# Kernel optimization log

Hardware: AMD Instinct MI355X
Metric: run time of the kernel (lower is better)

Reference implementation:

```python
import jax, jax.numpy as jnp
import numpy as np

B, I, H, O = 4096, 1024, 2048, 512  # batch, input_size, experts_out(hidden), experts_hidden(output)
E_SPEC, E_SH = 4, 4


def _experts(x, W1, b1, W2, b2):
    # x:[B,I], W1:[E,I,H], b1:[E,H], W2:[E,H,O], b2:[E,O] -> [E,B,O]
    # Expert: fc2(dropout(relu(fc1(x)))); dropout is identity in eval mode.
    h = jax.nn.relu(jnp.einsum('bi,eih->ebh', x, W1) + b1[:, None, :])
    return jnp.einsum('ebh,eho->ebo', h, W2) + b2[:, None, :]


def setup_inputs() -> dict:
    key = jax.random.key(0)
    ks = jax.random.split(key, 32)
    s = 0.02
    d = {}
    d['x_shared'] = jax.random.normal(ks[0], (B, I), jnp.float32)
    d['x_task1'] = jax.random.normal(ks[1], (B, I), jnp.float32)
    d['x_task2'] = jax.random.normal(ks[2], (B, I), jnp.float32)
    # expert params for shared / task1 / task2 groups
    for n, (grp, kbase) in enumerate([('sh', 3), ('t1', 8), ('t2', 13)]):
        E = E_SH if grp == 'sh' else E_SPEC
        d[f'w1_{grp}'] = jax.random.normal(ks[kbase], (E, I, H), jnp.float32) * s
        d[f'b1_{grp}'] = jnp.zeros((E, H), jnp.float32)
        d[f'w2_{grp}'] = jax.random.normal(ks[kbase + 1], (E, H, O), jnp.float32) * s
        d[f'b2_{grp}'] = jnp.zeros((E, O), jnp.float32)
    # gate params
    d['wg_sh'] = jax.random.normal(ks[20], (I, 2 * E_SPEC + E_SH), jnp.float32) * s
    d['bg_sh'] = jnp.zeros((2 * E_SPEC + E_SH,), jnp.float32)
    d['wg_t1'] = jax.random.normal(ks[21], (I, E_SPEC + E_SH), jnp.float32) * s
    d['bg_t1'] = jnp.zeros((E_SPEC + E_SH,), jnp.float32)
    d['wg_t2'] = jax.random.normal(ks[22], (I, E_SPEC + E_SH), jnp.float32) * s
    d['bg_t2'] = jnp.zeros((E_SPEC + E_SH,), jnp.float32)
    return d


def reference(x_shared, x_task1, x_task2,
              w1_sh, b1_sh, w2_sh, b2_sh,
              w1_t1, b1_t1, w2_t1, b2_t1,
              w1_t2, b1_t2, w2_t2, b2_t2,
              wg_sh, bg_sh, wg_t1, bg_t1, wg_t2, bg_t2):
    sh_o = _experts(x_shared, w1_sh, b1_sh, w2_sh, b2_sh)  # [Esh,B,O]
    t1_o = _experts(x_task1, w1_t1, b1_t1, w2_t1, b2_t1)   # [Esp,B,O]
    t2_o = _experts(x_task2, w1_t2, b1_t2, w2_t2, b2_t2)   # [Esp,B,O]

    g1 = jax.nn.softmax(x_task1 @ wg_t1 + bg_t1, axis=1)    # [B,Esp+Esh]
    g2 = jax.nn.softmax(x_task2 @ wg_t2 + bg_t2, axis=1)
    gs = jax.nn.softmax(x_shared @ wg_sh + bg_sh, axis=1)   # [B,2Esp+Esh]

    out1 = jnp.einsum('ebc,be->bc', jnp.concatenate([t1_o, sh_o], 0), g1)
    out2 = jnp.einsum('ebc,be->bc', jnp.concatenate([t2_o, sh_o], 0), g2)
    out_sh = jnp.einsum('ebc,be->bc', jnp.concatenate([t1_o, t2_o, sh_o], 0), gs)
    # if_last=False -> return [shared, task1, task2]
    return (out_sh, out1, out2)
```

## Files before the change

### kernel.cpp

```cpp
#include <hip/hip_runtime.h>

#define B_DIM 4096
#define I_DIM 1024
#define H_DIM 2048
#define O_DIM 512

typedef unsigned short ushort_t;
typedef unsigned long long ull_t;
typedef __attribute__((ext_vector_type(4))) float f32x4;
typedef __attribute__((ext_vector_type(8))) short bf16x8;
typedef __attribute__((ext_vector_type(8))) unsigned short u16x8;
typedef __attribute__((ext_vector_type(4))) unsigned short u16x4;

__device__ __forceinline__ unsigned short f2bf(float f) {
  union { float f; unsigned int u; } v; v.f = f;
  unsigned int u = v.u;
  u += 0x7fffu + ((u >> 16) & 1u);
  return (unsigned short)(u >> 16);
}
__device__ __forceinline__ float bf2f(unsigned short h) {
  union { unsigned int u; float f; } v; v.u = ((unsigned int)h) << 16;
  return v.f;
}

__device__ __forceinline__ void gld16(const void* g, void* l) {
  __builtin_amdgcn_global_load_lds(
      (const __attribute__((address_space(1))) unsigned int*)((ull_t)g),
      (__attribute__((address_space(3))) unsigned int*)((unsigned int)(ull_t)l),
      16, 0, 0);
}

__device__ __forceinline__ int swz_off(int row, int col) {
  int off = ((((row >> 4) << 1) + (col >> 5)) << 10) + ((row & 15) << 6) + ((col & 31) << 1);
  off ^= ((row >> 3) & 1) << 5;
  return off;
}

template <bool RELU>
__device__ __forceinline__ void gemm_core_256(
    const ushort_t* __restrict__ A,
    const ushort_t* __restrict__ Bt,
    const float*    __restrict__ bias,
    ushort_t*       __restrict__ C,
    int N, int K, int bm0, int bn0)
{
  __shared__ __align__(16) ushort_t sh[2][2][16384];

  const int tid  = threadIdx.x;
  const int lane = tid & 63;
  const int wave = tid >> 6;
  const int wm = wave >> 2, wn = wave & 3;
  const int r16 = lane & 15, kq = lane >> 4;

  int   loff[4];
  ull_t goffA[4], goffB[4];
#pragma unroll
  for (int r = 0; r < 4; ++r) {
    const int L = (r * 512 + tid) * 16;
    const int P = L ^ (((L >> 9) & 1) << 5);
    const int s = P >> 10;
    const int row = ((s >> 1) << 4) | ((P >> 6) & 15);
    const int col = ((s & 1) << 5) | (((P >> 4) & 3) << 3);
    loff[r]  = L;
    goffA[r] = (ull_t)(bm0 + row) * K + col;
    goffB[r] = (ull_t)(bn0 + row) * K + col;
  }
  const int NT = K >> 6;

  int offA[8][2], offB[4][2];
#pragma unroll
  for (int m = 0; m < 8; ++m)
#pragma unroll
    for (int ks = 0; ks < 2; ++ks)
      offA[m][ks] = swz_off(wm * 128 + m * 16 + r16, ks * 32 + kq * 8);
#pragma unroll
  for (int n = 0; n < 4; ++n)
#pragma unroll
    for (int ks = 0; ks < 2; ++ks)
      offB[n][ks] = swz_off(wn * 64 + n * 16 + r16, ks * 32 + kq * 8);

  f32x4 acc[8][4] = {};

  auto stageA = [&](int b, int kt) {
    const int k0 = kt << 6;
    char* baseA = (char*)&sh[b][0][0];
#pragma unroll
    for (int r = 0; r < 4; ++r) gld16(A + goffA[r] + k0, baseA + loff[r]);
  };
  auto stageB = [&](int b, int kt) {
    const int k0 = kt << 6;
    char* baseB = (char*)&sh[b][1][0];
#pragma unroll
    for (int r = 0; r < 4; ++r) gld16(Bt + goffB[r] + k0, baseB + loff[r]);
  };

  stageA(0, 0); stageB(0, 0);
  stageA(1, 1); stageB(1, 1);

  for (int kt = 0; kt < NT; ++kt) {
    const int b = kt & 1;
    const bool pre = (kt + 2 < NT);
    if (kt < NT - 1) asm volatile("s_waitcnt vmcnt(8)" ::: "memory");
    else             asm volatile("s_waitcnt vmcnt(0)" ::: "memory");
    __builtin_amdgcn_s_barrier();

    const char* tA = (const char*)&sh[b][0][0];
    const char* tB = (const char*)&sh[b][1][0];

    bf16x8 a0[4][2], a1[4][2], bf0[2][2], bf1[2][2];

#pragma unroll
    for (int m = 0; m < 4; ++m) {
      a0[m][0] = *(const bf16x8*)(tA + offA[m][0]);
      a0[m][1] = *(const bf16x8*)(tA + offA[m][1]);
    }
#pragma unroll
    for (int n = 0; n < 2; ++n) {
      bf0[n][0] = *(const bf16x8*)(tB + offB[n][0]);
      bf0[n][1] = *(const bf16x8*)(tB + offB[n][1]);
    }
    asm volatile("" ::: "memory");
    __builtin_amdgcn_s_barrier();
    asm volatile("s_waitcnt lgkmcnt(0)" ::: "memory");
    __builtin_amdgcn_sched_barrier(0);
    __builtin_amdgcn_s_setprio(1);
#pragma unroll
    for (int m = 0; m < 4; ++m)
#pragma unroll
      for (int n = 0; n < 2; ++n)
#pragma unroll
        for (int ks = 0; ks < 2; ++ks)
          acc[m][n] = __builtin_amdgcn_mfma_f32_16x16x32_bf16(a0[m][ks], bf0[n][ks], acc[m][n], 0, 0, 0);
    __builtin_amdgcn_s_setprio(0);
    asm volatile("" ::: "memory");
    __builtin_amdgcn_s_barrier();

#pragma unroll
    for (int n = 0; n < 2; ++n) {
      bf1[n][0] = *(const bf16x8*)(tB + offB[n + 2][0]);
      bf1[n][1] = *(const bf16x8*)(tB + offB[n + 2][1]);
    }
    asm volatile("" ::: "memory");
    __builtin_amdgcn_s_barrier();
    asm volatile("s_waitcnt lgkmcnt(0)" ::: "memory");
    __builtin_amdgcn_sched_barrier(0);
    __builtin_amdgcn_s_setprio(1);
#pragma unroll
    for (int m = 0; m < 4; ++m)
#pragma unroll
      for (int n = 0; n < 2; ++n)
#pragma unroll
        for (int ks = 0; ks < 2; ++ks)
          acc[m][n + 2] = __builtin_amdgcn_mfma_f32_16x16x32_bf16(a0[m][ks], bf1[n][ks], acc[m][n + 2], 0, 0, 0);
    __builtin_amdgcn_s_setprio(0);
    asm volatile("" ::: "memory");
    __builtin_amdgcn_s_barrier();

#pragma unroll
    for (int m = 0; m < 4; ++m) {
      a1[m][0] = *(const bf16x8*)(tA + offA[m + 4][0]);
      a1[m][1] = *(const bf16x8*)(tA + offA[m + 4][1]);
    }
    if (pre) stageB(b, kt + 2);
    asm volatile("" ::: "memory");
    __builtin_amdgcn_s_barrier();
    asm volatile("s_waitcnt lgkmcnt(0)" ::: "memory");
    __builtin_amdgcn_sched_barrier(0);
    __builtin_amdgcn_s_setprio(1);
#pragma unroll
    for (int m = 0; m < 4; ++m)
#pragma unroll
      for (int n = 0; n < 2; ++n)
#pragma unroll
        for (int ks = 0; ks < 2; ++ks)
          acc[m + 4][n + 2] = __builtin_amdgcn_mfma_f32_16x16x32_bf16(a1[m][ks], bf1[n][ks], acc[m + 4][n + 2], 0, 0, 0);
    __builtin_amdgcn_s_setprio(0);
    asm volatile("" ::: "memory");
    __builtin_amdgcn_s_barrier();

    if (pre) stageA(b, kt + 2);
    asm volatile("" ::: "memory");
    __builtin_amdgcn_s_barrier();
    __builtin_amdgcn_sched_barrier(0);
    __builtin_amdgcn_s_setprio(1);
#pragma unroll
    for (int m = 0; m < 4; ++m)
#pragma unroll
      for (int n = 0; n < 2; ++n)
#pragma unroll
        for (int ks = 0; ks < 2; ++ks)
          acc[m + 4][n] = __builtin_amdgcn_mfma_f32_16x16x32_bf16(a1[m][ks], bf0[n][ks], acc[m + 4][n], 0, 0, 0);
    __builtin_amdgcn_s_setprio(0);
    asm volatile("" ::: "memory");
    __builtin_amdgcn_s_barrier();
  }

  float bv[4];
#pragma unroll
  for (int n = 0; n < 4; ++n) bv[n] = bias[bn0 + wn * 64 + n * 16 + r16];
#pragma unroll
  for (int m = 0; m < 8; ++m) {
    const int row = bm0 + wm * 128 + m * 16 + kq * 4;
#pragma unroll
    for (int n = 0; n < 4; ++n) {
      const int col = bn0 + wn * 64 + n * 16 + r16;
#pragma unroll
      for (int j = 0; j < 4; ++j) {
        float v = acc[m][n][j] + bv[n];
        if (RELU) v = fmaxf(v, 0.f);
        C[(ull_t)(row + j) * N + col] = f2bf(v);
      }
    }
  }
}

__device__ __forceinline__ void xcd_swz(int& bx, int& by, int& bz) {
  const int gx = gridDim.x, gy = gridDim.y;
  const int total = gx * gy * gridDim.z;
  const int flat = blockIdx.x + gx * (blockIdx.y + gy * blockIdx.z);
  const int q = total >> 3;
  const int s = (flat & 7) * q + (flat >> 3);
  bx = s % gx;
  const int rest = s / gx;
  by = rest % gy;
  bz = rest / gy;
}

__global__ __launch_bounds__(512, 2) void gemm1_256_kernel(
    const ushort_t* __restrict__ xb,
    const ushort_t* __restrict__ w1t,
    const float* __restrict__ b1_t1, const float* __restrict__ b1_t2, const float* __restrict__ b1_sh,
    ushort_t* __restrict__ hbuf,
    int ebase)
{
  int bx, by, bz; xcd_swz(bx, by, bz);
  const int eg = ebase + bz;
  const ushort_t* A  = xb + (ull_t)(eg >> 2) * B_DIM * I_DIM;
  const ushort_t* Bt = w1t + (ull_t)bz * H_DIM * I_DIM;
  const float* bias = (eg < 4 ? b1_t1 : eg < 8 ? b1_t2 : b1_sh) + (ull_t)(eg & 3) * H_DIM;
  ushort_t* C = hbuf + (ull_t)bz * B_DIM * H_DIM;
  gemm_core_256<true>(A, Bt, bias, C, H_DIM, I_DIM, by * 256, bx * 256);
}

__global__ __launch_bounds__(512, 2) void gemm2_256_kernel(
    const ushort_t* __restrict__ hbuf,
    const ushort_t* __restrict__ w2t,
    const float* __restrict__ b2_t1, const float* __restrict__ b2_t2, const float* __restrict__ b2_sh,
    ushort_t* __restrict__ eout,
    int ebase)
{
  int bx, by, bz; xcd_swz(bx, by, bz);
  const int eg = ebase + bz;
  const ushort_t* A  = hbuf + (ull_t)bz * B_DIM * H_DIM;
  const ushort_t* Bt = w2t + (ull_t)bz * O_DIM * H_DIM;
  const float* bias = (eg < 4 ? b2_t1 : eg < 8 ? b2_t2 : b2_sh) + (ull_t)(eg & 3) * O_DIM;
  ushort_t* C = eout + (ull_t)eg * B_DIM * O_DIM;
  gemm_core_256<false>(A, Bt, bias, C, O_DIM, H_DIM, by * 256, bx * 256);
}

__global__ void tcast_kernel(const float* __restrict__ s_t1, const float* __restrict__ s_t2,
                             const float* __restrict__ s_sh, ushort_t* __restrict__ dst,
                             int R, int C, int ebase)
{
  __shared__ float tile[32][33];
  const int eg = ebase + blockIdx.z;
  const float* src = (eg < 4 ? s_t1 : eg < 8 ? s_t2 : s_sh) + (ull_t)(eg & 3) * R * C;
  ushort_t* d = dst + (ull_t)blockIdx.z * R * C;
  const int tx = threadIdx.x, ty = threadIdx.y;
  const int r0 = blockIdx.y * 32, c0 = blockIdx.x * 32;
#pragma unroll
  for (int i = 0; i < 32; i += 8)
    tile[ty + i][tx] = src[(ull_t)(r0 + ty + i) * C + c0 + tx];
  __syncthreads();
#pragma unroll
  for (int i = 0; i < 32; i += 8)
    d[(ull_t)(c0 + ty + i) * R + r0 + tx] = f2bf(tile[tx][ty + i]);
}

__global__ void cast_x_kernel(const float* __restrict__ xt1, const float* __restrict__ xt2,
                              const float* __restrict__ xsh, ushort_t* __restrict__ dst)
{
  const int slot = blockIdx.y;
  const float* src = slot == 0 ? xt1 : slot == 1 ? xt2 : xsh;
  const ull_t base = ((ull_t)blockIdx.x * 256 + threadIdx.x) * 8;
  const f32x4* s4 = (const f32x4*)(src + base);
  f32x4 a = s4[0], b = s4[1];
  u16x8 r;
  r[0] = f2bf(a[0]); r[1] = f2bf(a[1]); r[2] = f2bf(a[2]); r[3] = f2bf(a[3]);
  r[4] = f2bf(b[0]); r[5] = f2bf(b[1]); r[6] = f2bf(b[2]); r[7] = f2bf(b[3]);
  *(u16x8*)(dst + (ull_t)slot * B_DIM * I_DIM + base) = r;
}

__global__ void prep_gates_w_kernel(const float* __restrict__ wg_sh, const float* __restrict__ wg_t1,
                                    const float* __restrict__ wg_t2, ushort_t* __restrict__ wgtb)
{
  const int t = blockIdx.x;
  const float* src = t == 0 ? wg_sh : t == 1 ? wg_t1 : wg_t2;
  const int n = t == 0 ? 12 : 8;
  ushort_t* dst = wgtb + (ull_t)t * 16 * I_DIM;
  for (int i = threadIdx.x; i < 16 * (I_DIM / 8); i += blockDim.x) {
    const int c = i >> 7, j0 = (i & 127) * 8;
    u16x8 r;
#pragma unroll
    for (int k = 0; k < 8; ++k)
      r[k] = (c < n) ? f2bf(src[(ull_t)(j0 + k) * n + c]) : (ushort_t)0;
    *(u16x8*)(dst + (ull_t)c * I_DIM + j0) = r;
  }
}

__global__ __launch_bounds__(256, 2) void gates_mfma_kernel(
    const ushort_t* __restrict__ xb, const ushort_t* __restrict__ wgtb,
    const float* __restrict__ bg_sh, const float* __restrict__ bg_t1, const float* __restrict__ bg_t2,
    float* __restrict__ gates)
{
  __shared__ __align__(16) ushort_t As[128 * 32];
  const int task = blockIdx.y;
  const int slot = task == 0 ? 2 : task - 1;
  const int n = task == 0 ? 12 : 8;
  const float* bg = task == 0 ? bg_sh : task == 1 ? bg_t1 : bg_t2;
  float* out = task == 0 ? gates
             : task == 1 ? gates + (ull_t)B_DIM * 12
                         : gates + (ull_t)B_DIM * 20;
  const ushort_t* A  = xb + (ull_t)slot * B_DIM * I_DIM;
  const ushort_t* Bt = wgtb + (ull_t)task * 16 * I_DIM;

  const int tid = threadIdx.x, lane = tid & 63, wave = tid >> 6;
  const int brow = blockIdx.x * 128;
  const int r16 = lane & 15, kq = lane >> 4;

  f32x4 acc[2] = {};
  const int c0 = tid, c1 = tid + 256;
  const ull_t a_off0 = (ull_t)(brow + (c0 >> 2)) * I_DIM + (c0 & 3) * 8;
  const ull_t a_off1 = (ull_t)(brow + (c1 >> 2)) * I_DIM + (c1 & 3) * 8;

  for (int k0 = 0; k0 < I_DIM; k0 += 32) {
    gld16(A + a_off0 + k0, As + c0 * 8);
    gld16(A + a_off1 + k0, As + c1 * 8);
    __syncthreads();
    const bf16x8 bfr = *(const bf16x8*)(Bt + (ull_t)r16 * I_DIM + k0 + kq * 8);
    const bf16x8 af0 = *(const bf16x8*)(As + (wave * 32 + r16) * 32 + kq * 8);
    const bf16x8 af1 = *(const bf16x8*)(As + (wave * 32 + 16 + r16) * 32 + kq * 8);
    acc[0] = __builtin_amdgcn_mfma_f32_16x16x32_bf16(af0, bfr, acc[0], 0, 0, 0);
    acc[1] = __builtin_amdgcn_mfma_f32_16x16x32_bf16(af1, bfr, acc[1], 0, 0, 0);
    __syncthreads();
  }

  const float bv = (r16 < n) ? bg[r16] : 0.f;
#pragma unroll
  for (int m = 0; m < 2; ++m) {
#pragma unroll
    for (int j = 0; j < 4; ++j) {
      float v = (r16 < n) ? (acc[m][j] + bv) : -1e30f;
      float mx = v;
#pragma unroll
      for (int d = 1; d < 16; d <<= 1) mx = fmaxf(mx, __shfl_xor(mx, d));
      const float e = __expf(v - mx);
      float s = e;
#pragma unroll
      for (int d = 1; d < 16; d <<= 1) s += __shfl_xor(s, d);
      const int row = brow + wave * 32 + m * 16 + kq * 4 + j;
      if (r16 < n) out[(ull_t)row * n + r16] = e / s;
    }
  }
}

__global__ __launch_bounds__(256) void combine_kernel(
    const ushort_t* __restrict__ eout, const float* __restrict__ gates, float* __restrict__ out)
{
  const ull_t idx4 = (ull_t)blockIdx.x * 256 + threadIdx.x;
  const int b  = (int)(idx4 >> 7);
  const int o4 = ((int)idx4 & 127) * 4;
  const float* gs = gates + (ull_t)b * 12;
  const float* g1 = gates + (ull_t)B_DIM * 12 + (ull_t)b * 8;
  const float* g2 = gates + (ull_t)B_DIM * 20 + (ull_t)b * 8;
  float osh[4] = {0, 0, 0, 0}, o1[4] = {0, 0, 0, 0}, o2[4] = {0, 0, 0, 0};
#pragma unroll
  for (int j = 0; j < 12; ++j) {
    const u16x4 ev = *(const u16x4*)(eout + ((ull_t)j * B_DIM + b) * O_DIM + o4);
    const float wsh = gs[j];
    const float w1 = (j < 4) ? g1[j] : (j >= 8 ? g1[j - 4] : 0.f);
    const float w2 = (j < 4) ? 0.f : g2[j - 4];
#pragma unroll
    for (int t = 0; t < 4; ++t) {
      const float e = bf2f(ev[t]);
      osh[t] += wsh * e; o1[t] += w1 * e; o2[t] += w2 * e;
    }
  }
  const ull_t nBO = (ull_t)B_DIM * O_DIM;
  const ull_t obase = (ull_t)b * O_DIM + o4;
  f32x4 v0 = {osh[0], osh[1], osh[2], osh[3]};
  f32x4 v1 = {o1[0], o1[1], o1[2], o1[3]};
  f32x4 v2 = {o2[0], o2[1], o2[2], o2[3]};
  *(f32x4*)(out + obase) = v0;
  *(f32x4*)(out + nBO + obase) = v1;
  *(f32x4*)(out + 2 * nBO + obase) = v2;
}

extern "C" void kernel_launch(void* const* d_in, const int* in_sizes, int n_in,
                              void* d_out, int out_size, void* d_ws, size_t ws_size,
                              hipStream_t stream)
{
  const float* x_sh  = (const float*)d_in[0];
  const float* x_t1  = (const float*)d_in[1];
  const float* x_t2  = (const float*)d_in[2];
  const float* w1_sh = (const float*)d_in[3];
  const float* b1_sh = (const float*)d_in[4];
  const float* w2_sh = (const float*)d_in[5];
  const float* b2_sh = (const float*)d_in[6];
  const float* w1_t1 = (const float*)d_in[7];
  const float* b1_t1 = (const float*)d_in[8];
  const float* w2_t1 = (const float*)d_in[9];
  const float* b2_t1 = (const float*)d_in[10];
  const float* w1_t2 = (const float*)d_in[11];
  const float* b1_t2 = (const float*)d_in[12];
  const float* w2_t2 = (const float*)d_in[13];
  const float* b2_t2 = (const float*)d_in[14];
  const float* wg_sh = (const float*)d_in[15];
  const float* bg_sh = (const float*)d_in[16];
  const float* wg_t1 = (const float*)d_in[17];
  const float* bg_t1 = (const float*)d_in[18];
  const float* wg_t2 = (const float*)d_in[19];
  const float* bg_t2 = (const float*)d_in[20];

  char* p = (char*)d_ws;
  auto alloc = [&](size_t bytes) { char* r = p; p += (bytes + 255) & ~(size_t)255; return r; };

  ushort_t* xb    = (ushort_t*)alloc(3ull * B_DIM * I_DIM * 2);
  ushort_t* eout  = (ushort_t*)alloc(12ull * B_DIM * O_DIM * 2);
  float*    gates = (float*)alloc(28ull * B_DIM * 4);
  ushort_t* wgtb  = (ushort_t*)alloc(3ull * 16 * I_DIM * 2);

  const size_t used_fixed = (size_t)(p - (char*)d_ws);
  const size_t per_e = ((size_t)H_DIM * I_DIM + (size_t)O_DIM * H_DIM + (size_t)B_DIM * H_DIM) * 2 + 3 * 256;
  int eb = 1;
  if (ws_size > used_fixed + per_e) eb = (int)((ws_size - used_fixed) / per_e);
  if (eb > 12) eb = 12;
  if (eb < 1)  eb = 1;

  ushort_t* w1t  = (ushort_t*)alloc((size_t)eb * H_DIM * I_DIM * 2);
  ushort_t* w2t  = (ushort_t*)alloc((size_t)eb * O_DIM * H_DIM * 2);
  ushort_t* hbuf = (ushort_t*)alloc((size_t)eb * B_DIM * H_DIM * 2);

  cast_x_kernel<<<dim3(2048, 3), 256, 0, stream>>>(x_t1, x_t2, x_sh, xb);
  prep_gates_w_kernel<<<3, 256, 0, stream>>>(wg_sh, wg_t1, wg_t2, wgtb);
  gates_mfma_kernel<<<dim3(B_DIM / 128, 3), 256, 0, stream>>>(xb, wgtb, bg_sh, bg_t1, bg_t2, gates);
  for (int ebase = 0; ebase < 12; ebase += eb) {
    const int cnt = (12 - ebase < eb) ? (12 - ebase) : eb;
    tcast_kernel<<<dim3(H_DIM / 32, I_DIM / 32, cnt), dim3(32, 8), 0, stream>>>(
        w1_t1, w1_t2, w1_sh, w1t, I_DIM, H_DIM, ebase);
    tcast_kernel<<<dim3(O_DIM / 32, H_DIM / 32, cnt), dim3(32, 8), 0, stream>>>(
        w2_t1, w2_t2, w2_sh, w2t, H_DIM, O_DIM, ebase);
    gemm1_256_kernel<<<dim3(H_DIM / 256, B_DIM / 256, cnt), 512, 0, stream>>>(
        xb, w1t, b1_t1, b1_t2, b1_sh, hbuf, ebase);
    gemm2_256_kernel<<<dim3(O_DIM / 256, B_DIM / 256, cnt), 512, 0, stream>>>(
        hbuf, w2t, b2_t1, b2_t2, b2_sh, eout, ebase);
  }
  combine_kernel<<<dim3((B_DIM * O_DIM / 4) / 256), 256, 0, stream>>>(eout, gates, (float*)d_out);
}
```

Measured before the change: 443.2 us.

## Templatize GEMM tiles, use 256x128 tiles for gemm2, vectorize transpose-cast stores

Turns the GEMM core into a template over the wave grid and per-wave MFMA repeats, so gemm2 can use 256x128 tiles (a 4x2 wave grid) and launch twice as many blocks. With only 512 output columns, the old 256x256 tiling gave gemm2 few blocks. The weight transpose-cast kernel now handles 64-row tiles and writes 16-byte vector stores instead of scalar 2-byte stores. In exchange, gemm2 re-reads each A tile more often and its LDS and register footprint changes.

```diff
diff --git a/kernel.cpp b/kernel.cpp
--- a/kernel.cpp
+++ b/kernel.cpp
@@ -36,62 +36,81 @@
   return off;
 }
 
-template <bool RELU>
-__device__ __forceinline__ void gemm_core_256(
+template <bool RELU, int WM, int WN, int MR, int NR>
+__device__ __forceinline__ void gemm_core(
     const ushort_t* __restrict__ A,
     const ushort_t* __restrict__ Bt,
     const float*    __restrict__ bias,
     ushort_t*       __restrict__ C,
     int N, int K, int bm0, int bn0)
 {
-  __shared__ __align__(16) ushort_t sh[2][2][16384];
+  constexpr int BM = WM * MR * 16;
+  constexpr int BN = WN * NR * 16;
+  constexpr int CA = BM / 64;
+  constexpr int CB = BN / 64;
+  constexpr int NTH = WM * WN * 64;
+  constexpr int MH = MR / 2, NH = NR / 2;
+  constexpr int ABYTES = BM * 128;
+  constexpr int BBYTES = BN * 128;
+  constexpr int VM = CA + CB;
+
+  __shared__ __align__(16) char lds[2 * (ABYTES + BBYTES)];
 
   const int tid  = threadIdx.x;
   const int lane = tid & 63;
   const int wave = tid >> 6;
-  const int wm = wave >> 2, wn = wave & 3;
+  const int wm = wave / WN, wn = wave % WN;
   const int r16 = lane & 15, kq = lane >> 4;
 
-  int   loff[4];
-  ull_t goffA[4], goffB[4];
-#pragma unroll
-  for (int r = 0; r < 4; ++r) {
-    const int L = (r * 512 + tid) * 16;
+  int loffA[CA]; ull_t goffA[CA];
+  int loffB[CB]; ull_t goffB[CB];
+#pragma unroll
+  for (int r = 0; r < CA; ++r) {
+    const int L = (r * NTH + tid) * 16;
     const int P = L ^ (((L >> 9) & 1) << 5);
     const int s = P >> 10;
     const int row = ((s >> 1) << 4) | ((P >> 6) & 15);
     const int col = ((s & 1) << 5) | (((P >> 4) & 3) << 3);
-    loff[r]  = L;
+    loffA[r] = L;
     goffA[r] = (ull_t)(bm0 + row) * K + col;
+  }
+#pragma unroll
+  for (int r = 0; r < CB; ++r) {
+    const int L = (r * NTH + tid) * 16;
+    const int P = L ^ (((L >> 9) & 1) << 5);
+    const int s = P >> 10;
+    const int row = ((s >> 1) << 4) | ((P >> 6) & 15);
+    const int col = ((s & 1) << 5) | (((P >> 4) & 3) << 3);
+    loffB[r] = L;
     goffB[r] = (ull_t)(bn0 + row) * K + col;
   }
   const int NT = K >> 6;
 
-  int offA[8][2], offB[4][2];
-#pragma unroll
-  for (int m = 0; m < 8; ++m)
+  int offA[MR][2], offB[NR][2];
+#pragma unroll
+  for (int m = 0; m < MR; ++m)
 #pragma unroll
     for (int ks = 0; ks < 2; ++ks)
-      offA[m][ks] = swz_off(wm * 128 + m * 16 + r16, ks * 32 + kq * 8);
-#pragma unroll
-  for (int n = 0; n < 4; ++n)
+      offA[m][ks] = swz_off(wm * MR * 16 + m * 16 + r16, ks * 32 + kq * 8);
+#pragma unroll
+  for (int n = 0; n < NR; ++n)
 #pragma unroll
     for (int ks = 0; ks < 2; ++ks)
-      offB[n][ks] = swz_off(wn * 64 + n * 16 + r16, ks * 32 + kq * 8);
-
-  f32x4 acc[8][4] = {};
+      offB[n][ks] = swz_off(wn * NR * 16 + n * 16 + r16, ks * 32 + kq * 8);
+
+  f32x4 acc[MR][NR] = {};
 
   auto stageA = [&](int b, int kt) {
+    char* base = lds + b * (ABYTES + BBYTES);
     const int k0 = kt << 6;
-    char* baseA = (char*)&sh[b][0][0];
-#pragma unroll
-    for (int r = 0; r < 4; ++r) gld16(A + goffA[r] + k0, baseA + loff[r]);
+#pragma unroll
+    for (int r = 0; r < CA; ++r) gld16(A + goffA[r] + k0, base + loffA[r]);
   };
   auto stageB = [&](int b, int kt) {
+    char* base = lds + b * (ABYTES + BBYTES) + ABYTES;
     const int k0 = kt << 6;
-    char* baseB = (char*)&sh[b][1][0];
-#pragma unroll
-    for (int r = 0; r < 4; ++r) gld16(Bt + goffB[r] + k0, baseB + loff[r]);
+#pragma unroll
+    for (int r = 0; r < CB; ++r) gld16(Bt + goffB[r] + k0, base + loffB[r]);
   };
 
   stageA(0, 0); stageB(0, 0);
@@ -100,24 +119,27 @@
   for (int kt = 0; kt < NT; ++kt) {
     const int b = kt & 1;
     const bool pre = (kt + 2 < NT);
-    if (kt < NT - 1) asm volatile("s_waitcnt vmcnt(8)" ::: "memory");
-    else             asm volatile("s_waitcnt vmcnt(0)" ::: "memory");
-    __builtin_amdgcn_s_barrier();
-
-    const char* tA = (const char*)&sh[b][0][0];
-    const char* tB = (const char*)&sh[b][1][0];
-
-    bf16x8 a0[4][2], a1[4][2], bf0[2][2], bf1[2][2];
-
-#pragma unroll
-    for (int m = 0; m < 4; ++m) {
-      a0[m][0] = *(const bf16x8*)(tA + offA[m][0]);
-      a0[m][1] = *(const bf16x8*)(tA + offA[m][1]);
-    }
-#pragma unroll
-    for (int n = 0; n < 2; ++n) {
-      bf0[n][0] = *(const bf16x8*)(tB + offB[n][0]);
-      bf0[n][1] = *(const bf16x8*)(tB + offB[n][1]);
+    if (kt < NT - 1) {
+      if constexpr (VM == 8)      asm volatile("s_waitcnt vmcnt(8)" ::: "memory");
+      else if constexpr (VM == 6) asm volatile("s_waitcnt vmcnt(6)" ::: "memory");
+      else                        asm volatile("s_waitcnt vmcnt(0)" ::: "memory");
+    } else                        asm volatile("s_waitcnt vmcnt(0)" ::: "memory");
+    __builtin_amdgcn_s_barrier();
+
+    const char* tA = lds + b * (ABYTES + BBYTES);
+    const char* tB = tA + ABYTES;
+
+    bf16x8 a_lo[MH][2], a_hi[MH][2], b_lo[NH][2], b_hi[NH][2];
+
+#pragma unroll
+    for (int m = 0; m < MH; ++m) {
+      a_lo[m][0] = *(const bf16x8*)(tA + offA[m][0]);
+      a_lo[m][1] = *(const bf16x8*)(tA + offA[m][1]);
+    }
+#pragma unroll
+    for (int n = 0; n < NH; ++n) {
+      b_lo[n][0] = *(const bf16x8*)(tB + offB[n][0]);
+      b_lo[n][1] = *(const bf16x8*)(tB + offB[n][1]);
     }
     asm volatile("" ::: "memory");
     __builtin_amdgcn_s_barrier();
@@ -125,20 +147,20 @@
     __builtin_amdgcn_sched_barrier(0);
     __builtin_amdgcn_s_setprio(1);
 #pragma unroll
-    for (int m = 0; m < 4; ++m)
-#pragma unroll
-      for (int n = 0; n < 2; ++n)
+    for (int m = 0; m < MH; ++m)
+#pragma unroll
+      for (int n = 0; n < NH; ++n)
 #pragma unroll
         for (int ks = 0; ks < 2; ++ks)
-          acc[m][n] = __builtin_amdgcn_mfma_f32_16x16x32_bf16(a0[m][ks], bf0[n][ks], acc[m][n], 0, 0, 0);
+          acc[m][n] = __builtin_amdgcn_mfma_f32_16x16x32_bf16(a_lo[m][ks], b_lo[n][ks], acc[m][n], 0, 0, 0);
     __builtin_amdgcn_s_setprio(0);
     asm volatile("" ::: "memory");
     __builtin_amdgcn_s_barrier();
 
 #pragma unroll
-    for (int n = 0; n < 2; ++n) {
-      bf1[n][0] = *(const bf16x8*)(tB + offB[n + 2][0]);
-      bf1[n][1] = *(const bf16x8*)(tB + offB[n + 2][1]);
+    for (int n = 0; n < NH; ++n) {
+      b_hi[n][0] = *(const bf16x8*)(tB + offB[n + NH][0]);
+      b_hi[n][1] = *(const bf16x8*)(tB + offB[n + NH][1]);
     }
     asm volatile("" ::: "memory");
     __builtin_amdgcn_s_barrier();
@@ -146,20 +168,20 @@
     __builtin_amdgcn_sched_barrier(0);
     __builtin_amdgcn_s_setprio(1);
 #pragma unroll
-    for (int m = 0; m < 4; ++m)
-#pragma unroll
-      for (int n = 0; n < 2; ++n)
+    for (int m = 0; m < MH; ++m)
+#pragma unroll
+      for (int n = 0; n < NH; ++n)
 #pragma unroll
         for (int ks = 0; ks < 2; ++ks)
-          acc[m][n + 2] = __builtin_amdgcn_mfma_f32_16x16x32_bf16(a0[m][ks], bf1[n][ks], acc[m][n + 2], 0, 0, 0);
+          acc[m][n + NH] = __builtin_amdgcn_mfma_f32_16x16x32_bf16(a_lo[m][ks], b_hi[n][ks], acc[m][n + NH], 0, 0, 0);
     __builtin_amdgcn_s_setprio(0);
     asm volatile("" ::: "memory");
     __builtin_amdgcn_s_barrier();
 
 #pragma unroll
-    for (int m = 0; m < 4; ++m) {
-      a1[m][0] = *(const bf16x8*)(tA + offA[m + 4][0]);
-      a1[m][1] = *(const bf16x8*)(tA + offA[m + 4][1]);
+    for (int m = 0; m < MH; ++m) {
+      a_hi[m][0] = *(const bf16x8*)(tA + offA[m + MH][0]);
+      a_hi[m][1] = *(const bf16x8*)(tA + offA[m + MH][1]);
     }
     if (pre) stageB(b, kt + 2);
     asm volatile("" ::: "memory");
@@ -168,12 +190,12 @@
     __builtin_amdgcn_sched_barrier(0);
     __builtin_amdgcn_s_setprio(1);
 #pragma unroll
-    for (int m = 0; m < 4; ++m)
-#pragma unroll
-      for (int n = 0; n < 2; ++n)
+    for (int m = 0; m < MH; ++m)
+#pragma unroll
+      for (int n = 0; n < NH; ++n)
 #pragma unroll
         for (int ks = 0; ks < 2; ++ks)
-          acc[m + 4][n + 2] = __builtin_amdgcn_mfma_f32_16x16x32_bf16(a1[m][ks], bf1[n][ks], acc[m + 4][n + 2], 0, 0, 0);
+          acc[m + MH][n + NH] = __builtin_amdgcn_mfma_f32_16x16x32_bf16(a_hi[m][ks], b_hi[n][ks], acc[m + MH][n + NH], 0, 0, 0);
     __builtin_amdgcn_s_setprio(0);
     asm volatile("" ::: "memory");
     __builtin_amdgcn_s_barrier();
@@ -184,26 +206,26 @@
     __builtin_amdgcn_sched_barrier(0);
     __builtin_amdgcn_s_setprio(1);
 #pragma unroll
-    for (int m = 0; m < 4; ++m)
-#pragma unroll
-      for (int n = 0; n < 2; ++n)
+    for (int m = 0; m < MH; ++m)
+#pragma unroll
+      for (int n = 0; n < NH; ++n)
 #pragma unroll
         for (int ks = 0; ks < 2; ++ks)
-          acc[m + 4][n] = __builtin_amdgcn_mfma_f32_16x16x32_bf16(a1[m][ks], bf0[n][ks], acc[m + 4][n], 0, 0, 0);
+          acc[m + MH][n] = __builtin_amdgcn_mfma_f32_16x16x32_bf16(a_hi[m][ks], b_lo[n][ks], acc[m + MH][n], 0, 0, 0);
     __builtin_amdgcn_s_setprio(0);
     asm volatile("" ::: "memory");
     __builtin_amdgcn_s_barrier();
   }
 
-  float bv[4];
-#pragma unroll
-  for (int n = 0; n < 4; ++n) bv[n] = bias[bn0 + wn * 64 + n * 16 + r16];
-#pragma unroll
-  for (int m = 0; m < 8; ++m) {
-    const int row = bm0 + wm * 128 + m * 16 + kq * 4;
-#pragma unroll
-    for (int n = 0; n < 4; ++n) {
-      const int col = bn0 + wn * 64 + n * 16 + r16;
+  float bv[NR];
+#pragma unroll
+  for (int n = 0; n < NR; ++n) bv[n] = bias[bn0 + wn * NR * 16 + n * 16 + r16];
+#pragma unroll
+  for (int m = 0; m < MR; ++m) {
+    const int row = bm0 + wm * MR * 16 + m * 16 + kq * 4;
+#pragma unroll
+    for (int n = 0; n < NR; ++n) {
+      const int col = bn0 + wn * NR * 16 + n * 16 + r16;
 #pragma unroll
       for (int j = 0; j < 4; ++j) {
         float v = acc[m][n][j] + bv[n];
@@ -239,7 +261,7 @@
   const ushort_t* Bt = w1t + (ull_t)bz * H_DIM * I_DIM;
   const float* bias = (eg < 4 ? b1_t1 : eg < 8 ? b1_t2 : b1_sh) + (ull_t)(eg & 3) * H_DIM;
   ushort_t* C = hbuf + (ull_t)bz * B_DIM * H_DIM;
-  gemm_core_256<true>(A, Bt, bias, C, H_DIM, I_DIM, by * 256, bx * 256);
+  gemm_core<true, 2, 4, 8, 4>(A, Bt, bias, C, H_DIM, I_DIM, by * 256, bx * 256);
 }
 
 __global__ __launch_bounds__(512, 2) void gemm2_256_kernel(
@@ -255,26 +277,29 @@
   const ushort_t* Bt = w2t + (ull_t)bz * O_DIM * H_DIM;
   const float* bias = (eg < 4 ? b2_t1 : eg < 8 ? b2_t2 : b2_sh) + (ull_t)(eg & 3) * O_DIM;
   ushort_t* C = eout + (ull_t)eg * B_DIM * O_DIM;
-  gemm_core_256<false>(A, Bt, bias, C, O_DIM, H_DIM, by * 256, bx * 256);
-}
-
-__global__ void tcast_kernel(const float* __restrict__ s_t1, const float* __restrict__ s_t2,
-                             const float* __restrict__ s_sh, ushort_t* __restrict__ dst,
-                             int R, int C, int ebase)
-{
-  __shared__ float tile[32][33];
+  gemm_core<false, 4, 2, 4, 4>(A, Bt, bias, C, O_DIM, H_DIM, by * 256, bx * 128);
+}
+
+__global__ void tcast64_kernel(const float* __restrict__ s_t1, const float* __restrict__ s_t2,
+                               const float* __restrict__ s_sh, ushort_t* __restrict__ dst,
+                               int R, int C, int ebase)
+{
+  __shared__ float tile[64][33];
   const int eg = ebase + blockIdx.z;
   const float* src = (eg < 4 ? s_t1 : eg < 8 ? s_t2 : s_sh) + (ull_t)(eg & 3) * R * C;
   ushort_t* d = dst + (ull_t)blockIdx.z * R * C;
   const int tx = threadIdx.x, ty = threadIdx.y;
-  const int r0 = blockIdx.y * 32, c0 = blockIdx.x * 32;
-#pragma unroll
-  for (int i = 0; i < 32; i += 8)
-    tile[ty + i][tx] = src[(ull_t)(r0 + ty + i) * C + c0 + tx];
+  const int r0 = blockIdx.y * 64, c0 = blockIdx.x * 32;
+#pragma unroll
+  for (int i = 0; i < 64; i += 8)
+    tile[i + ty][tx] = src[(ull_t)(r0 + i + ty) * C + c0 + tx];
   __syncthreads();
-#pragma unroll
-  for (int i = 0; i < 32; i += 8)
-    d[(ull_t)(c0 + ty + i) * R + r0 + tx] = f2bf(tile[tx][ty + i]);
+  const int tid = ty * 32 + tx;
+  const int c = tid >> 3, q = tid & 7;
+  u16x8 rv;
+#pragma unroll
+  for (int k = 0; k < 8; ++k) rv[k] = f2bf(tile[q * 8 + k][c]);
+  *(u16x8*)(d + (ull_t)(c0 + c) * R + r0 + q * 8) = rv;
 }
 
 __global__ void cast_x_kernel(const float* __restrict__ xt1, const float* __restrict__ xt2,
@@ -446,13 +471,13 @@
   gates_mfma_kernel<<<dim3(B_DIM / 128, 3), 256, 0, stream>>>(xb, wgtb, bg_sh, bg_t1, bg_t2, gates);
   for (int ebase = 0; ebase < 12; ebase += eb) {
     const int cnt = (12 - ebase < eb) ? (12 - ebase) : eb;
-    tcast_kernel<<<dim3(H_DIM / 32, I_DIM / 32, cnt), dim3(32, 8), 0, stream>>>(
+    tcast64_kernel<<<dim3(H_DIM / 32, I_DIM / 64, cnt), dim3(32, 8), 0, stream>>>(
         w1_t1, w1_t2, w1_sh, w1t, I_DIM, H_DIM, ebase);
-    tcast_kernel<<<dim3(O_DIM / 32, H_DIM / 32, cnt), dim3(32, 8), 0, stream>>>(
+    tcast64_kernel<<<dim3(O_DIM / 32, H_DIM / 64, cnt), dim3(32, 8), 0, stream>>>(
         w2_t1, w2_t2, w2_sh, w2t, H_DIM, O_DIM, ebase);
     gemm1_256_kernel<<<dim3(H_DIM / 256, B_DIM / 256, cnt), 512, 0, stream>>>(
         xb, w1t, b1_t1, b1_t2, b1_sh, hbuf, ebase);
-    gemm2_256_kernel<<<dim3(O_DIM / 256, B_DIM / 256, cnt), 512, 0, stream>>>(
+    gemm2_256_kernel<<<dim3(O_DIM / 128, B_DIM / 256, cnt), 512, 0, stream>>>(
         hbuf, w2t, b2_t1, b2_t2, b2_sh, eout, ebase);
   }
   combine_kernel<<<dim3((B_DIM * O_DIM / 4) / 256), 256, 0, stream>>>(eout, gates, (float*)d_out);
```

New measurement: 432.1 us. -2.5%, faster.
